# Kernel tuning notes

Measured on AMD Instinct MI355X. Metric: run time of the kernel, lower is better.

## Reference

```python
import jax, jax.numpy as jnp
import numpy as np

N, H, W, C = 2048, 64, 64, 8
E, G, M = 4, 512, 512            # experts, group size per class, max_output_cells
CELLS = [128, 256, 384, 512]     # classes_config.values()


def setup_inputs() -> dict:
    key = jax.random.key(0)
    k = jax.random.split(key, 6)
    inputs = jax.random.normal(k[0], (N, H, W, C), dtype=jnp.float32)
    # input_config: class -> sample indices (equal partition of the batch)
    indices = jnp.arange(N, dtype=jnp.int32).reshape(E, G)
    W1 = jax.random.normal(k[1], (E, 1, 1, C, C), dtype=jnp.float32) * 0.1
    W3 = jax.random.normal(k[2], (E, 3, 3, C, C), dtype=jnp.float32) * 0.1
    Wskip = jax.random.normal(k[3], (E, 1, 1, C, 2 * C), dtype=jnp.float32) * 0.1
    Wd = jax.random.normal(k[4], (E, 2 * C, M), dtype=jnp.float32) * 0.1
    # zero-pad each expert's output beyond its num_output_layer_cells
    cell_mask = (jnp.arange(M)[None, :] < jnp.asarray(CELLS)[:, None]).astype(jnp.float32)
    return {"inputs": inputs, "indices": indices, "W1": W1, "W3": W3,
            "Wskip": Wskip, "Wd": Wd, "cell_mask": cell_mask}


def _conv(x, w):
    # x: [G,H,W,Cin], w: [kh,kw,Cin,Cout] -> [G,H,W,Cout], SAME padding
    return jax.lax.conv_general_dilated(x, w, (1, 1), 'SAME',
                                        dimension_numbers=('NHWC', 'HWIO', 'NHWC'))


def _expert(x, w1, w3, ws, wd, mask):
    # Hybrid inception + skip: parallel 1x1/3x3 branches, channel concat, 1x1-projected skip
    b1 = jax.nn.relu(_conv(x, w1))           # [G,H,W,C]
    b2 = jax.nn.relu(_conv(x, w3))           # [G,H,W,C]
    y = jnp.concatenate([b1, b2], axis=-1) + _conv(x, ws)  # [G,H,W,2C]
    pooled = y.mean(axis=(1, 2))             # [G,2C]
    return (pooled @ wd) * mask[None, :]     # [G,M], padded to max_output_cells


def reference(inputs, indices, W1, W3, Wskip, Wd, cell_mask):
    # class-indexed gather: [E,G,H,W,C]
    groups = inputs[indices]
    # dispatch each group to its expert, vmapped over experts
    outs = jax.vmap(_expert)(groups, W1, W3, Wskip, Wd, cell_mask)  # [E,G,M]
    # concat along batch in class order (matches outputs.extend + tf.concat axis=0)
    return outs.reshape(E * G, M)
```

## Files before the change

### kernel.cpp

```cpp
#include <hip/hip_runtime.h>
#include <hip/hip_bf16.h>

#define MM    512
#define NROWS 36
#define ROWSZ (66 * 8)

typedef short bf16x8 __attribute__((ext_vector_type(8)));
typedef float f32x4  __attribute__((ext_vector_type(4)));

static __device__ inline short f2bf(float f) {
    __hip_bfloat16 h = __float2bfloat16(f);
    return *reinterpret_cast<short*>(&h);
}

__global__ __launch_bounds__(256, 4)
void conv_moe_mfma(const float* __restrict__ x,
                   const int*   __restrict__ idx,
                   const float* __restrict__ W1,
                   const float* __restrict__ W3,
                   const float* __restrict__ Wsk,
                   const float* __restrict__ Wd,
                   const float* __restrict__ cmask,
                   float*       __restrict__ out)
{
    __shared__ short xbf[NROWS][66][8];
    __shared__ float red[4][16];
    __shared__ float redx[4][8];
    __shared__ float rsum[16];
    __shared__ float rsumx[8];
    __shared__ float pooledS[16];

    const int b    = blockIdx.x;
    const int e    = b >> 9;
    const int tid  = threadIdx.x;
    const int lane = tid & 63;
    const int wid  = tid >> 6;
    const int g    = lane >> 4;
    const int p    = lane & 15;
    const int CB   = wid << 4;

    const int samp = idx[b];
    const float* xb = x + (size_t)samp * 32768;

    const float* w3 = W3 + e * 576;
    const float* w1 = W1 + e * 64;
    bf16x8 bf0, bf1, bf2, bid;
    #pragma unroll
    for (int j = 0; j < 8; ++j) {
        float v0 = 0.f, v1 = 0.f, v2 = 0.f, vi = 0.f;
        if (p >= 8) {
            v0 = w3[g * 64 + j * 8 + (p - 8)];
            v1 = w3[(4 + g) * 64 + j * 8 + (p - 8)];
            if (g == 0) v2 = w3[8 * 64 + j * 8 + (p - 8)];
        } else {
            if (g == 0) { v1 = w1[j * 8 + p]; vi = (j == p) ? 1.f : 0.f; }
        }
        bf0[j] = f2bf(v0); bf1[j] = f2bf(v1); bf2[j] = f2bf(v2); bid[j] = f2bf(vi);
    }

    const int d0 = g / 3;
    const int d1 = (4 + g) / 3;
    const int c0 = (CB + p + (g % 3)) * 8;
    const int c1 = (CB + p + ((4 + g) % 3)) * 8;
    const int c2 = (CB + p + 2) * 8;

    if (tid < 72) {
        const int rr = tid >> 1, side = tid & 1;
        bf16x8 zv = {0,0,0,0,0,0,0,0};
        *(bf16x8*)&xbf[rr][side ? 65 : 0][0] = zv;
    }

    const float4 z4 = make_float4(0.f, 0.f, 0.f, 0.f);
    float4 ra[5][2];

    #pragma unroll
    for (int j5 = 0; j5 < 5; ++j5) {
        const int j = j5 * 256 + tid;
        ra[j5][0] = z4; ra[j5][1] = z4;
        if (j < 1152) {
            const int lrow = j >> 6, c = j & 63;
            const int r = lrow - 1;
            if (r >= 0) {
                const float4* s4 = (const float4*)(xb + (((r << 6) + c) << 3));
                ra[j5][0] = s4[0];
                ra[j5][1] = s4[1];
            }
        }
    }
    #pragma unroll
    for (int j5 = 0; j5 < 5; ++j5) {
        const int j = j5 * 256 + tid;
        if (j < 1152) {
            const int lrow = j >> 6, c = j & 63;
            bf16x8 v;
            v[0] = f2bf(ra[j5][0].x); v[1] = f2bf(ra[j5][0].y);
            v[2] = f2bf(ra[j5][0].z); v[3] = f2bf(ra[j5][0].w);
            v[4] = f2bf(ra[j5][1].x); v[5] = f2bf(ra[j5][1].y);
            v[6] = f2bf(ra[j5][1].z); v[7] = f2bf(ra[j5][1].w);
            *(bf16x8*)&xbf[lrow][c + 1][0] = v;
        }
    }
    __syncthreads();

    f32x4 ssum = {0.f, 0.f, 0.f, 0.f};
    f32x4 acc2 = {0.f, 0.f, 0.f, 0.f};

    #pragma unroll 1
    for (int s = 0; s < 4; ++s) {
        if (s < 3) {
            const int rbase = 16 * s + 17;
            #pragma unroll
            for (int j5 = 0; j5 < 4; ++j5) {
                const int j = j5 * 256 + tid;
                const int lrow = j >> 6, c = j & 63;
                const int r = rbase + lrow;
                ra[j5][0] = z4; ra[j5][1] = z4;
                if (r < 64) {
                    const float4* s4 = (const float4*)(xb + (((r << 6) + c) << 3));
                    ra[j5][0] = s4[0];
                    ra[j5][1] = s4[1];
                }
            }
        }

        {
            int tb = 16 * s;
            const int sbase = (tb >= NROWS) ? tb - NROWS : tb;
            const short* base = &xbf[0][0][0];
            #pragma unroll 2
            for (int rl = 0; rl < 16; ++rl) {
                const int srl = sbase + rl;
                int t0 = srl + d0; t0 = (t0 >= NROWS) ? t0 - NROWS : t0;
                int t1 = srl + d1; t1 = (t1 >= NROWS) ? t1 - NROWS : t1;
                int t2 = srl + 2;  t2 = (t2 >= NROWS) ? t2 - NROWS : t2;
                const bf16x8 a0 = *(const bf16x8*)(base + t0 * ROWSZ + c0);
                const bf16x8 a1 = *(const bf16x8*)(base + t1 * ROWSZ + c1);
                bf16x8 a2 = {0,0,0,0,0,0,0,0};
                if (g == 0)
                    a2 = *(const bf16x8*)(base + t2 * ROWSZ + c2);
                f32x4 d = {0.f, 0.f, 0.f, 0.f};
                d = __builtin_amdgcn_mfma_f32_16x16x32_bf16(a0, bf0, d, 0, 0, 0);
                d = __builtin_amdgcn_mfma_f32_16x16x32_bf16(a1, bf1, d, 0, 0, 0);
                d = __builtin_amdgcn_mfma_f32_16x16x32_bf16(a2, bf2, d, 0, 0, 0);
                acc2 = __builtin_amdgcn_mfma_f32_16x16x32_bf16(a1, bid, acc2, 0, 0, 0);
                ssum[0] += fmaxf(d[0], 0.f);
                ssum[1] += fmaxf(d[1], 0.f);
                ssum[2] += fmaxf(d[2], 0.f);
                ssum[3] += fmaxf(d[3], 0.f);
            }
        }

        if (s < 3) {
            int wt = 16 * s + 18;
            const int wbase = (wt >= NROWS) ? wt - NROWS : wt;
            #pragma unroll
            for (int j5 = 0; j5 < 4; ++j5) {
                const int j = j5 * 256 + tid;
                const int lrow = j >> 6, c = j & 63;
                int ws = wbase + lrow; ws = (ws >= NROWS) ? ws - NROWS : ws;
                bf16x8 v;
                v[0] = f2bf(ra[j5][0].x); v[1] = f2bf(ra[j5][0].y);
                v[2] = f2bf(ra[j5][0].z); v[3] = f2bf(ra[j5][0].w);
                v[4] = f2bf(ra[j5][1].x); v[5] = f2bf(ra[j5][1].y);
                v[6] = f2bf(ra[j5][1].z); v[7] = f2bf(ra[j5][1].w);
                *(bf16x8*)&xbf[ws][c + 1][0] = v;
            }
            __syncthreads();
        }
    }

    float scon = ssum[0] + ssum[1] + ssum[2] + ssum[3];
    float sxs  = acc2[0] + acc2[1] + acc2[2] + acc2[3];
    scon += __shfl_xor(scon, 16);
    scon += __shfl_xor(scon, 32);
    sxs  += __shfl_xor(sxs, 16);
    sxs  += __shfl_xor(sxs, 32);
    if (lane < 16) red[wid][lane]  = scon;
    if (lane < 8)  redx[wid][lane] = sxs;
    __syncthreads();
    if (tid < 16) rsum[tid]  = (red[0][tid] + red[1][tid] + red[2][tid] + red[3][tid]) * (1.f / 4096.f);
    if (tid < 8)  rsumx[tid] = (redx[0][tid] + redx[1][tid] + redx[2][tid] + redx[3][tid]) * (1.f / 4096.f);
    __syncthreads();

    if (tid < 16) {
        float acc = rsum[tid];
        #pragma unroll
        for (int ci = 0; ci < 8; ++ci)
            acc += rsumx[ci] * Wsk[e * 128 + ci * 16 + tid];
        pooledS[tid] = acc;
    }
    __syncthreads();

    const float* wd = Wd + (size_t)e * 16 * MM;
    const float* cm = cmask + e * MM;
    #pragma unroll 1
    for (int m = tid; m < MM; m += 256) {
        float acc = 0.f;
        #pragma unroll
        for (int k = 0; k < 16; ++k) acc += pooledS[k] * wd[k * MM + m];
        out[(size_t)b * MM + m] = acc * cm[m];
    }
}

extern "C" void kernel_launch(void* const* d_in, const int* in_sizes, int n_in,
                              void* d_out, int out_size, void* d_ws, size_t ws_size,
                              hipStream_t stream) {
    const float* x    = (const float*)d_in[0];
    const int*   idx  = (const int*)  d_in[1];
    const float* W1   = (const float*)d_in[2];
    const float* W3   = (const float*)d_in[3];
    const float* Wsk  = (const float*)d_in[4];
    const float* Wd   = (const float*)d_in[5];
    const float* cmsk = (const float*)d_in[6];
    float* out = (float*)d_out;

    conv_moe_mfma<<<2048, 256, 0, stream>>>(x, idx, W1, W3, Wsk, Wd, cmsk, out);
}
```

Measured before the change: 57.56 us.

## Shrink LDS row ring to 18-row buffer with halo copy between stages

Replaces the 36-row circular LDS buffer with an 18-row linear buffer. After each 16-row stage, the two halo rows are copied back to the top and the next 16 rows are written below them. This removes the modulo row-index arithmetic in the inner MFMA loop, and the third A operand is now loaded unconditionally, relying on zero weights for the lanes that do not need it. It also halves the LDS footprint, which could allow more resident blocks, at the cost of an extra barrier and a small copy per stage.

```diff
diff --git a/kernel.cpp b/kernel.cpp
--- a/kernel.cpp
+++ b/kernel.cpp
@@ -1,8 +1,7 @@
 #include <hip/hip_runtime.h>
 #include <hip/hip_bf16.h>
 
-#define MM    512
-#define NROWS 36
+#define MM 512
 #define ROWSZ (66 * 8)
 
 typedef short bf16x8 __attribute__((ext_vector_type(8)));
@@ -23,7 +22,7 @@
                    const float* __restrict__ cmask,
                    float*       __restrict__ out)
 {
-    __shared__ short xbf[NROWS][66][8];
+    __shared__ short xbf[18][66][8];
     __shared__ float red[4][16];
     __shared__ float redx[4][8];
     __shared__ float rsum[16];
@@ -58,13 +57,12 @@
         bf0[j] = f2bf(v0); bf1[j] = f2bf(v1); bf2[j] = f2bf(v2); bid[j] = f2bf(vi);
     }
 
-    const int d0 = g / 3;
-    const int d1 = (4 + g) / 3;
-    const int c0 = (CB + p + (g % 3)) * 8;
-    const int c1 = (CB + p + ((4 + g) % 3)) * 8;
-    const int c2 = (CB + p + 2) * 8;
-
-    if (tid < 72) {
+    int off0, off1, off2;
+    { const int t = g;     const int dr = t / 3, dc = t % 3; off0 = (dr * 66 + CB + p + dc) * 8; }
+    { const int t = 4 + g; const int dr = t / 3, dc = t % 3; off1 = (dr * 66 + CB + p + dc) * 8; }
+    {                      const int dr = 2,     dc = 2;     off2 = (dr * 66 + CB + p + dc) * 8; }
+
+    if (tid < 36) {
         const int rr = tid >> 1, side = tid & 1;
         bf16x8 zv = {0,0,0,0,0,0,0,0};
         *(bf16x8*)&xbf[rr][side ? 65 : 0][0] = zv;
@@ -108,7 +106,7 @@
     #pragma unroll 1
     for (int s = 0; s < 4; ++s) {
         if (s < 3) {
-            const int rbase = 16 * s + 17;
+            const int rbase = 16 * (s + 1) + 1;
             #pragma unroll
             for (int j5 = 0; j5 < 4; ++j5) {
                 const int j = j5 * 256 + tid;
@@ -124,20 +122,13 @@
         }
 
         {
-            int tb = 16 * s;
-            const int sbase = (tb >= NROWS) ? tb - NROWS : tb;
             const short* base = &xbf[0][0][0];
             #pragma unroll 2
             for (int rl = 0; rl < 16; ++rl) {
-                const int srl = sbase + rl;
-                int t0 = srl + d0; t0 = (t0 >= NROWS) ? t0 - NROWS : t0;
-                int t1 = srl + d1; t1 = (t1 >= NROWS) ? t1 - NROWS : t1;
-                int t2 = srl + 2;  t2 = (t2 >= NROWS) ? t2 - NROWS : t2;
-                const bf16x8 a0 = *(const bf16x8*)(base + t0 * ROWSZ + c0);
-                const bf16x8 a1 = *(const bf16x8*)(base + t1 * ROWSZ + c1);
-                bf16x8 a2 = {0,0,0,0,0,0,0,0};
-                if (g == 0)
-                    a2 = *(const bf16x8*)(base + t2 * ROWSZ + c2);
+                const short* rbase2 = base + rl * ROWSZ;
+                const bf16x8 a0 = *(const bf16x8*)(rbase2 + off0);
+                const bf16x8 a1 = *(const bf16x8*)(rbase2 + off1);
+                const bf16x8 a2 = *(const bf16x8*)(rbase2 + off2);
                 f32x4 d = {0.f, 0.f, 0.f, 0.f};
                 d = __builtin_amdgcn_mfma_f32_16x16x32_bf16(a0, bf0, d, 0, 0, 0);
                 d = __builtin_amdgcn_mfma_f32_16x16x32_bf16(a1, bf1, d, 0, 0, 0);
@@ -150,20 +141,25 @@
             }
         }
 
+        bf16x8 rcopy;
+        if (s < 3 && tid < 128)
+            rcopy = *(const bf16x8*)&xbf[16 + (tid >> 6)][(tid & 63) + 1][0];
+
+        __syncthreads();
+
         if (s < 3) {
-            int wt = 16 * s + 18;
-            const int wbase = (wt >= NROWS) ? wt - NROWS : wt;
+            if (tid < 128)
+                *(bf16x8*)&xbf[tid >> 6][(tid & 63) + 1][0] = rcopy;
             #pragma unroll
             for (int j5 = 0; j5 < 4; ++j5) {
                 const int j = j5 * 256 + tid;
-                const int lrow = j >> 6, c = j & 63;
-                int ws = wbase + lrow; ws = (ws >= NROWS) ? ws - NROWS : ws;
+                const int lrow = 2 + (j >> 6), c = j & 63;
                 bf16x8 v;
                 v[0] = f2bf(ra[j5][0].x); v[1] = f2bf(ra[j5][0].y);
                 v[2] = f2bf(ra[j5][0].z); v[3] = f2bf(ra[j5][0].w);
                 v[4] = f2bf(ra[j5][1].x); v[5] = f2bf(ra[j5][1].y);
                 v[6] = f2bf(ra[j5][1].z); v[7] = f2bf(ra[j5][1].w);
-                *(bf16x8*)&xbf[ws][c + 1][0] = v;
+                *(bf16x8*)&xbf[lrow][c + 1][0] = v;
             }
             __syncthreads();
         }
```

After: 52.30 us. 1.1x faster.
